# Optimization experiments

Hardware: AMD Instinct MI355X
Metric: run time of the kernel (lower is better)

Reference implementation:

```python
import jax, jax.numpy as jnp
import numpy as np

B, L, H, S2V = 32, 1024, 256, 256
STEP = 1          # HP_SLSTM_step window size
EPS = 1e-3        # LayerNorm eps (added to std, torch-style unbiased std)
NUM_LAYERS = 4
# LayerNorm param row indices in ln_a/ln_b:
# 0..5 -> word gates f1,f2,f3,f4,i,o ; 6 gd ; 7 go ; 8 gf ; 9 gi ; 10 gg


def _ln(x, a, b):
    # torch LayerNorm variant: unbiased std, eps added to std (not var)
    mean = x.mean(-1, keepdims=True)
    d = x - mean
    std = jnp.sqrt((d * d).sum(-1, keepdims=True) / (x.shape[-1] - 1))
    return a * d / (std + EPS) + b


def setup_inputs() -> dict:
    key = jax.random.key(0)
    ks = jax.random.split(key, 16)
    p = lambda k, shp: 0.1 * jax.random.normal(k, shp, dtype=jnp.float32)
    return {
        "word_inputs": jax.random.normal(ks[0], (B, L, H), dtype=jnp.float32),
        "sent_embeddings": jax.random.normal(ks[1], (B, S2V), dtype=jnp.float32),
        "mask": jnp.ones((B, L), dtype=jnp.float32),
        "h0": jax.random.uniform(ks[2], (B, L, H), minval=-0.05, maxval=0.05, dtype=jnp.float32),
        "c0": jax.random.uniform(ks[3], (B, L, H), minval=-0.05, maxval=0.05, dtype=jnp.float32),
        "Wx_g": p(ks[4], (6, H, H)),
        "Wh_g": p(ks[5], (6, 2 * H, H)),
        "Wi_g": p(ks[6], (6, H, H)),
        "Wd_g": p(ks[7], (6, H, H)),
        "b_g": p(ks[8], (6, H)),
        "gWx": p(ks[9], (4, H, H)),   # dummy gates d,i,o,f
        "gWh": p(ks[10], (4, H, H)),
        "gWg": p(ks[11], (4, S2V, H)),  # d,i,o,g
        "gb": p(ks[12], (4, H)),
        "ln_a": jnp.ones((11, H), dtype=jnp.float32),
        "ln_b": jnp.zeros((11, H), dtype=jnp.float32),
        "num_layers": NUM_LAYERS,
    }


def _win_sums(t):
    # sum of left-shifted (before) and right-shifted (after) neighbor states
    bef = jnp.zeros_like(t)
    aft = jnp.zeros_like(t)
    for s in range(1, STEP + 1):
        bef = bef + jnp.pad(t[:, :-s], ((0, 0), (s, 0), (0, 0)))
        aft = aft + jnp.pad(t[:, s:], ((0, 0), (0, s), (0, 0)))
    return bef.reshape(-1, t.shape[-1]), aft.reshape(-1, t.shape[-1])


def reference(word_inputs, sent_embeddings, mask, h0, c0, Wx_g, Wh_g, Wi_g,
              Wd_g, b_g, gWx, gWh, gWg, gb, ln_a, ln_b, num_layers):
    Bs, Ls, Hs = word_inputs.shape
    seq_mask = mask[..., None]                      # (B,L,1)
    msm = (mask * 1e25 - 1e25)[..., None]           # softmax mask (B,L,1)
    emb_h = (word_inputs * seq_mask).reshape(-1, Hs)  # fixed word embedding states
    emb_c = emb_h
    h = h0 * seq_mask
    c = c0 * seq_mask
    dh = h.mean(axis=1)                             # dummy (sentence) node (B,H)
    dc = c.mean(axis=1)

    for _ in range(num_layers):
        comb = h.mean(axis=1)                       # (B,H)
        rh = h.reshape(-1, Hs)                      # (B*L,H)
        tdh = (dh[:, None, :] * seq_mask).reshape(-1, Hs)
        tdc = (dc[:, None, :] * seq_mask).reshape(-1, Hs)

        # --- dummy (sentence-level) node gates ---
        gd = jax.nn.sigmoid(_ln(dh @ gWx[0] + sent_embeddings @ gWg[0] + comb @ gWh[0] + gb[0], ln_a[6], ln_b[6]))
        gi = jax.nn.sigmoid(_ln(dh @ gWx[1] + sent_embeddings @ gWg[1] + comb @ gWh[1], ln_a[9], ln_b[9]) + gb[1])  # bias outside LN, as in source
        gg = sent_embeddings @ gWg[3]
        go = jax.nn.sigmoid(_ln(dh @ gWx[2] + sent_embeddings @ gWg[2] + comb @ gWh[2] + gb[2], ln_a[7], ln_b[7]))
        gf = jax.nn.sigmoid(_ln(tdh @ gWx[3] + rh @ gWh[3] + gb[3], ln_a[8], ln_b[8]))
        gf = gf.reshape(Bs, Ls, Hs) + msm
        scores = jax.nn.softmax(jnp.concatenate([gf, gd[:, None, :], gi[:, None, :]], axis=1), axis=1)
        f_w = scores[:, :Ls]
        d_w = scores[:, Ls]
        i_w = scores[:, Ls + 1]
        dc_new = jnp.sum(f_w * c, axis=1) + d_w * dc + i_w * jnp.tanh(_ln(gg, ln_a[10], ln_b[10]))
        dh_new = go * jnp.tanh(dc_new)

        # --- word node gates (windowed message passing) ---
        hb, ha = _win_sums(h)
        cb, ca = _win_sums(c)
        cat_h = jnp.concatenate([hb, ha], axis=1)   # (B*L, 2H)
        pre = (jnp.einsum('nh,ghk->gnk', emb_h, Wx_g)
               + jnp.einsum('nc,gck->gnk', cat_h, Wh_g)
               + jnp.einsum('nh,ghk->gnk', rh, Wi_g)
               + jnp.einsum('nh,ghk->gnk', tdh, Wd_g)
               + b_g[:, None, :])                   # (6, B*L, H)
        gates = jax.nn.sigmoid(_ln(pre, ln_a[:6, None, :], ln_b[:6, None, :]))
        five = jax.nn.softmax(gates[:5], axis=0)    # normalize f1..f4,i
        f1, f2, f3, f4, i_t = five
        o_t = gates[5]
        c_new = cb * f1 + ca * f2 + emb_c * f3 + tdc * f4 + c.reshape(-1, Hs) * i_t
        h_new = o_t * jnp.tanh(c_new)
        h = h_new.reshape(Bs, Ls, Hs) * seq_mask
        c = c_new.reshape(Bs, Ls, Hs) * seq_mask
        dh, dc = dh_new, dc_new
    return h
```

## Files before the change

### kernel.cpp

```cpp
#include <hip/hip_runtime.h>
#include <cstddef>

#define Bz 32
#define Lz 1024
#define Hz 256
#define Nz (Bz*Lz)
#define NHz ((size_t)Nz*Hz)
#define BHz (Bz*Hz)
#define EPSz 1e-3f
#define NLAYERS 4
#define NCH 64
#define NTC 112
#define CHR 16384

typedef __bf16 bf8_t __attribute__((ext_vector_type(8)));
typedef __bf16 bf4_t __attribute__((ext_vector_type(4)));
typedef float  f4_t  __attribute__((ext_vector_type(4)));

__device__ inline float sigmoidf(float x){ return 1.f/(1.f+expf(-x)); }
__device__ inline float fsig(float x){ return __builtin_amdgcn_rcpf(1.f + __expf(-x)); }
__device__ inline float ftanh(float x){ return 1.f - 2.f*__builtin_amdgcn_rcpf(__expf(2.f*x)+1.f); }

template<int C>
__device__ inline float dppadd(float v){
  int t = __builtin_amdgcn_update_dpp(0, __builtin_bit_cast(int, v), C, 0xf, 0xf, true);
  return v + __builtin_bit_cast(float, t);
}
__device__ inline float dppsum16(float v){
  v = dppadd<0x111>(v);
  v = dppadd<0x112>(v);
  v = dppadd<0x114>(v);
  v = dppadd<0x118>(v);
  return v;
}

__device__ inline void gl_lds16(const void* g, void* l){
  __builtin_amdgcn_global_load_lds(
      (const __attribute__((address_space(1))) void*)g,
      (__attribute__((address_space(3))) void*)l, 16, 0, 0);
}

__device__ inline float2 block_sum2(float a, float b, float* red){
  #pragma unroll
  for (int off=32; off; off>>=1){ a += __shfl_down(a,off,64); b += __shfl_down(b,off,64); }
  int w = threadIdx.x>>6;
  __syncthreads();
  if ((threadIdx.x&63)==0){ red[w]=a; red[4+w]=b; }
  __syncthreads();
  return make_float2(red[0]+red[1]+red[2]+red[3], red[4]+red[5]+red[6]+red[7]);
}

__device__ inline float ln_block(float v, const float* la, const float* lb, int t, float* red){
  float2 ss = block_sum2(v, v*v, red);
  float mean = ss.x*(1.f/Hz);
  float var  = (ss.y - (float)Hz*mean*mean)*(1.f/(Hz-1));
  float isd  = 1.f/(sqrtf(fmaxf(var,0.f))+EPSz);
  return la[t]*(v-mean)*isd + lb[t];
}

__global__ void k_initb(const float* __restrict__ word, const float* __restrict__ h0,
                        const float* __restrict__ c0, const float* __restrict__ mask,
                        __bf16* __restrict__ xe, __bf16* __restrict__ h, __bf16* __restrict__ c){
  int tid = blockIdx.x*256 + threadIdx.x;
  int n = tid >> 5; int c8 = (tid & 31)*8;
  float m = mask[n];
  size_t off = (size_t)n*Hz + c8;
  const float4* wv = (const float4*)(word + off);
  float4 w0 = wv[0], w1 = wv[1];
  bf8_t o;
  o[0]=(__bf16)(w0.x*m); o[1]=(__bf16)(w0.y*m); o[2]=(__bf16)(w0.z*m); o[3]=(__bf16)(w0.w*m);
  o[4]=(__bf16)(w1.x*m); o[5]=(__bf16)(w1.y*m); o[6]=(__bf16)(w1.z*m); o[7]=(__bf16)(w1.w*m);
  *(bf8_t*)(xe + off) = o;
  const float4* hv = (const float4*)(h0 + off);
  float4 a0 = hv[0], a1 = hv[1];
  o[0]=(__bf16)(a0.x*m); o[1]=(__bf16)(a0.y*m); o[2]=(__bf16)(a0.z*m); o[3]=(__bf16)(a0.w*m);
  o[4]=(__bf16)(a1.x*m); o[5]=(__bf16)(a1.y*m); o[6]=(__bf16)(a1.z*m); o[7]=(__bf16)(a1.w*m);
  *(bf8_t*)(h + off) = o;
  const float4* cv = (const float4*)(c0 + off);
  float4 b0 = cv[0], b1 = cv[1];
  o[0]=(__bf16)(b0.x*m); o[1]=(__bf16)(b0.y*m); o[2]=(__bf16)(b0.z*m); o[3]=(__bf16)(b0.w*m);
  o[4]=(__bf16)(b1.x*m); o[5]=(__bf16)(b1.y*m); o[6]=(__bf16)(b1.z*m); o[7]=(__bf16)(b1.w*m);
  *(bf8_t*)(c + off) = o;
}

__global__ void k_packWt(const float* __restrict__ Wx, const float* __restrict__ Wh,
                         const float* __restrict__ Wi, const float* __restrict__ gWh3,
                         __bf16* __restrict__ Wt, __bf16* __restrict__ zbuf){
  int tid = blockIdx.x*256 + threadIdx.x;
  if (tid < 128) zbuf[tid] = (__bf16)0.f;
  int col = tid >> 7;
  int k0  = (tid & 127) << 3;
  if (col >= 1792) return;
  int g = col >> 8, cg = col & 255;
  int seg = k0 >> 8, kl0 = k0 & 255;
  bf8_t o;
  #pragma unroll
  for (int j=0;j<8;j++){
    int kl = kl0 + j;
    float v = 0.f;
    if (g < 6){
      if (seg==0)      v = Wx[((size_t)g*256 + kl)*256 + cg];
      else if (seg==1) v = Wh[((size_t)g*512 + kl)*256 + cg];
      else if (seg==2) v = Wh[((size_t)g*512 + 256 + kl)*256 + cg];
      else             v = Wi[((size_t)g*256 + kl)*256 + cg];
    } else {
      if (seg==3)      v = gWh3[(size_t)kl*256 + cg];
    }
    o[j] = (__bf16)v;
  }
  *(bf8_t*)(Wt + (size_t)col*1024 + k0) = o;
}

__global__ void k_meanpb(const __bf16* __restrict__ x, float* __restrict__ part){
  int b = blockIdx.x, ch = blockIdx.y, t = threadIdx.x;
  const __bf16* p = x + ((size_t)b*Lz + ch*128)*Hz + t;
  float s = 0.f;
  #pragma unroll 4
  for (int l=0;l<128;l++) s += (float)p[(size_t)l*Hz];
  part[(b*8+ch)*Hz + t] = s;
}
__global__ void k_comb8(const float* __restrict__ part, float* __restrict__ o){
  int b = blockIdx.x, t = threadIdx.x;
  float s = 0.f;
  #pragma unroll
  for (int ch=0;ch<8;ch++) s += part[(b*8+ch)*Hz + t];
  o[b*Hz+t] = s*(1.f/Lz);
}

__global__ __launch_bounds__(256) void k_small(
    const float* __restrict__ dh, const float* __restrict__ comb, const float* __restrict__ sent,
    const float* __restrict__ gWx, const float* __restrict__ gWh, const float* __restrict__ gWg,
    const float* __restrict__ gb, const float* __restrict__ Wd_g,
    const float* __restrict__ ln_a, const float* __restrict__ ln_b,
    float* __restrict__ gd, float* __restrict__ gi, float* __restrict__ go,
    float* __restrict__ tgg, float* __restrict__ dhWd7){
  int b = blockIdx.x, which = blockIdx.y, t = threadIdx.x;
  __shared__ float sdh[Hz], sse[Hz], sco[Hz];
  __shared__ float red[8];
  sdh[t]=dh[b*Hz+t]; sse[t]=sent[b*Hz+t]; sco[t]=comb[b*Hz+t];
  __syncthreads();
  float acc=0.f;
  if (which < 3){
    const float* W0 = gWx + which*Hz*Hz;
    const float* W1 = gWg + which*Hz*Hz;
    const float* W2 = gWh + which*Hz*Hz;
    for (int k=0;k<Hz;k++) acc += sdh[k]*W0[k*Hz+t] + sse[k]*W1[k*Hz+t] + sco[k]*W2[k*Hz+t];
    if (which==0){
      float r = ln_block(acc + gb[0*Hz+t], ln_a+6*Hz, ln_b+6*Hz, t, red);
      gd[b*Hz+t] = sigmoidf(r);
    } else if (which==1){
      float r = ln_block(acc, ln_a+9*Hz, ln_b+9*Hz, t, red);
      gi[b*Hz+t] = sigmoidf(r + gb[1*Hz+t]);
    } else {
      float r = ln_block(acc + gb[2*Hz+t], ln_a+7*Hz, ln_b+7*Hz, t, red);
      go[b*Hz+t] = sigmoidf(r);
    }
  } else if (which == 3){
    const float* W = gWg + 3*Hz*Hz;
    for (int k=0;k<Hz;k++) acc += sse[k]*W[k*Hz+t];
    float r = ln_block(acc, ln_a+10*Hz, ln_b+10*Hz, t, red);
    tgg[b*Hz+t] = tanhf(r);
  } else if (which == 4){
    const float* W = gWx + 3*Hz*Hz;
    for (int k=0;k<Hz;k++) acc += sdh[k]*W[k*Hz+t];
    dhWd7[(6*Bz + b)*Hz + t] = acc;
  } else {
    int g = which-5;
    const float* W = Wd_g + g*Hz*Hz;
    for (int k=0;k<Hz;k++) acc += sdh[k]*W[k*Hz+t];
    dhWd7[(g*Bz + b)*Hz + t] = acc;
  }
}

__global__ __launch_bounds__(256) void k_gemm(
    const __bf16* __restrict__ xe, const __bf16* __restrict__ h,
    const __bf16* __restrict__ Wt, const __bf16* __restrict__ zbuf,
    __bf16* __restrict__ pre, int n_base){
  __shared__ __align__(16) __bf16 sA[2][128*64];
  __shared__ __align__(16) __bf16 sB[2][128*64];
  int t = threadIdx.x;
  int w = t>>6, lane = t&63;
  int m16 = lane&15, p = lane>>4;
  int bx = blockIdx.x, by = blockIdx.y;
  int row0 = n_base + bx*128;
  int coltile = by*128;

  f4_t acc[4][4];
  #pragma unroll
  for (int i=0;i<4;i++)
    #pragma unroll
    for (int j=0;j<4;j++) acc[i][j] = (f4_t){0.f,0.f,0.f,0.f};

  int srr = t>>3;
  int sck = t&7;
  int arow = (w&1)*64 + m16;
  int brow = (w>>1)*64 + m16;
  int swz  = m16 & 7;

  auto STAGE = [&](int kk, int buf){
    int seg = kk>>2;
    int kloc = (kk&3)*64;
    #pragma unroll
    for (int it=0; it<4; ++it){
      int drow = it*32 + srr;
      int sc = (sck ^ (drow&7)) << 3;
      int r = row0 + drow;
      const __bf16* asrc;
      if (seg==0)      asrc = xe + (size_t)r*Hz + kloc + sc;
      else if (seg==3) asrc = h + (size_t)r*Hz + kloc + sc;
      else if (seg==1) asrc = ((r&1023)==0)    ? zbuf : h + ((size_t)(r-1)*Hz + kloc + sc);
      else             asrc = ((r&1023)==1023) ? zbuf : h + ((size_t)(r+1)*Hz + kloc + sc);
      gl_lds16(asrc, &sA[buf][drow*64 + sck*8]);
      const __bf16* bsrc = Wt + (size_t)(coltile + drow)*1024 + seg*256 + kloc + sc;
      gl_lds16(bsrc, &sB[buf][drow*64 + sck*8]);
    }
  };

  int kk_s = (by >= 12) ? 12 : 0;
  STAGE(kk_s, 0);
  __syncthreads();
  int cur = 0;
  #pragma unroll 1
  for (int kk=kk_s; kk<16; ++kk){
    if (kk < 15) STAGE(kk+1, cur^1);
    const char* Ab = (const char*)sA[cur];
    const char* Bb = (const char*)sB[cur];
    #pragma unroll
    for (int kb=0; kb<2; ++kb){
      bf8_t a[4], bb[4];
      int cofs = ((kb*4 + p) ^ swz) << 4;
      #pragma unroll
      for (int tr=0;tr<4;tr++)
        a[tr] = *(const bf8_t*)(Ab + (arow + tr*16)*128 + cofs);
      #pragma unroll
      for (int tc=0;tc<4;tc++)
        bb[tc] = *(const bf8_t*)(Bb + (brow + tc*16)*128 + cofs);
      #pragma unroll
      for (int tr=0;tr<4;tr++)
        #pragma unroll
        for (int tc=0;tc<4;tc++)
          acc[tr][tc] = __builtin_amdgcn_mfma_f32_16x16x32_bf16(a[tr], bb[tc], acc[tr][tc], 0, 0, 0);
    }
    __syncthreads();
    cur ^= 1;
  }

  int trg0 = (bx*128 + (w&1)*64) >> 4;
  int tcg0 = (coltile + (w>>1)*64) >> 4;
  #pragma unroll
  for (int tr=0;tr<4;tr++){
    #pragma unroll
    for (int tc=0;tc<4;tc++){
      size_t tile = (size_t)(trg0+tr)*NTC + (tcg0+tc);
      bf4_t o;
      o[0]=(__bf16)acc[tr][tc][0]; o[1]=(__bf16)acc[tr][tc][1];
      o[2]=(__bf16)acc[tr][tc][2]; o[3]=(__bf16)acc[tr][tc][3];
      *(bf4_t*)(pre + tile*256 + lane*4) = o;
    }
  }
}

__global__ __launch_bounds__(1024) void k_epi(
    const __bf16* __restrict__ pre, const __bf16* __restrict__ xe,
    const __bf16* __restrict__ cc, const float* __restrict__ mask,
    const float* __restrict__ dhWd7, const float* __restrict__ b_g,
    const float* __restrict__ gb3, const float* __restrict__ ln_a, const float* __restrict__ ln_b,
    const float* __restrict__ dc,
    float* __restrict__ outf, __bf16* __restrict__ hn, __bf16* __restrict__ cn,
    float* __restrict__ pm, float* __restrict__ ps, float* __restrict__ pn,
    int n_base, int last){
  __shared__ float sred_s[16][7][16];
  __shared__ float sred_q[16][7][16];
  __shared__ float smean[7][16];
  __shared__ float sisd[7][16];
  __shared__ float hsh[16*260];
  int t = threadIdx.x;
  int n0 = n_base + blockIdx.x*16;
  int b = n0 >> 10;
  int w16 = t>>6, lane = t&63, m16 = lane&15, p = lane>>4;
  int col = w16*16 + m16;
  size_t trk = blockIdx.x;

  bf4_t pv[7];
  float wd[7], bg[7], la[7], lb[7];
  #pragma unroll
  for (int g=0; g<7; ++g){
    size_t tile = trk*NTC + g*16 + w16;
    pv[g] = *(const bf4_t*)(pre + tile*256 + lane*4);
    wd[g] = dhWd7[(g*Bz + b)*Hz + col];
    bg[g] = (g<6) ? b_g[g*Hz + col] : gb3[col];
    int lnr = (g<6) ? g : 8;
    la[g] = ln_a[lnr*Hz+col]; lb[g] = ln_b[lnr*Hz+col];
  }
  float msk4[4], cvv[4], cb4[4], ca4[4], em4[4];
  #pragma unroll
  for (int reg=0; reg<4; ++reg){
    int n2 = n0 + p*4 + reg;
    int l2 = n2 & 1023;
    msk4[reg] = mask[n2];
    cvv[reg] = (float)cc[(size_t)n2*Hz + col];
    cb4[reg] = (l2==0)    ? 0.f : (float)cc[(size_t)(n2-1)*Hz + col];
    ca4[reg] = (l2==1023) ? 0.f : (float)cc[(size_t)(n2+1)*Hz + col];
    em4[reg] = (float)xe[(size_t)n2*Hz + col];
  }
  float tdc = dc[b*Hz + col];

  float acc[7][4];
  #pragma unroll
  for (int g=0; g<7; ++g){
    float s_r[4], q_r[4];
    #pragma unroll
    for (int reg=0; reg<4; ++reg){
      float x = (float)pv[g][reg] + msk4[reg]*wd[g] + bg[g];
      acc[g][reg] = x;
      s_r[reg] = dppsum16(x);
      q_r[reg] = dppsum16(x*x);
    }
    if (m16==15){
      #pragma unroll
      for (int reg=0; reg<4; ++reg){
        sred_s[w16][g][p*4+reg] = s_r[reg];
        sred_q[w16][g][p*4+reg] = q_r[reg];
      }
    }
  }
  __syncthreads();

  if (t < 112){
    int g = t>>4, row = t&15;
    float ss=0.f, qq=0.f;
    #pragma unroll
    for (int ww=0; ww<16; ++ww){
      ss += sred_s[ww][g][row];
      qq += sred_q[ww][g][row];
    }
    float mean = ss*(1.f/Hz);
    float var  = (qq - (float)Hz*mean*mean)*(1.f/(Hz-1));
    smean[g][row] = mean;
    sisd[g][row]  = __builtin_amdgcn_rcpf(sqrtf(fmaxf(var,0.f))+EPSz);
  }
  __syncthreads();

  #pragma unroll
  for (int g=0; g<7; ++g){
    #pragma unroll
    for (int reg=0; reg<4; ++reg){
      int row = p*4+reg;
      acc[g][reg] = fsig(la[g]*(acc[g][reg]-smean[g][row])*sisd[g][row] + lb[g]);
    }
  }

  {
    float mm = -1e30f, gfv[4];
    #pragma unroll
    for (int reg=0; reg<4; ++reg){
      float gv = acc[6][reg] + (msk4[reg]*1e25f - 1e25f);
      gfv[reg] = gv;
      mm = fmaxf(mm, gv);
    }
    float ss=0.f, nn=0.f;
    #pragma unroll
    for (int reg=0; reg<4; ++reg){
      float e = __expf(gfv[reg]-mm);
      ss += e; nn += e*cvv[reg];
    }
    #pragma unroll
    for (int off=16; off<64; off<<=1){
      float mo = __shfl_xor(mm, off, 64);
      float so = __shfl_xor(ss, off, 64);
      float no = __shfl_xor(nn, off, 64);
      float mN = fmaxf(mm, mo);
      float ea = __expf(mm-mN), eb = __expf(mo-mN);
      ss = ss*ea + so*eb; nn = nn*ea + no*eb; mm = mN;
    }
    if (p==0){
      int ch = (n0 >> 4) & (NCH-1);
      int idx = (b*NCH + ch)*Hz + col;
      pm[idx]=mm; ps[idx]=ss; pn[idx]=nn;
    }
  }

  float cnv[4];
  #pragma unroll
  for (int reg=0; reg<4; ++reg){
    float msk = msk4[reg];
    float g0=acc[0][reg], g1=acc[1][reg], g2=acc[2][reg], g3=acc[3][reg], g4=acc[4][reg];
    float m5 = fmaxf(fmaxf(fmaxf(g0,g1),fmaxf(g2,g3)),g4);
    float e0=__expf(g0-m5), e1=__expf(g1-m5), e2=__expf(g2-m5), e3=__expf(g3-m5), e4=__expf(g4-m5);
    float inv = __builtin_amdgcn_rcpf(e0+e1+e2+e3+e4);
    float cnew = (cb4[reg]*e0 + ca4[reg]*e1 + em4[reg]*e2 + (tdc*msk)*e3 + cvv[reg]*e4)*inv;
    float hv = acc[5][reg]*ftanh(cnew);
    hsh[(p*4+reg)*260 + col] = hv*msk;
    cnv[reg] = cnew*msk;
  }
  __syncthreads();
  {
    int row = t>>6, c4 = lane*4;
    int n = n0 + row;
    const float* src = hsh + row*260 + c4;
    float v0=src[0], v1=src[1], v2=src[2], v3=src[3];
    if (last){
      *(float4*)(outf + (size_t)n*Hz + c4) = make_float4(v0,v1,v2,v3);
    } else {
      bf4_t o; o[0]=(__bf16)v0; o[1]=(__bf16)v1; o[2]=(__bf16)v2; o[3]=(__bf16)v3;
      *(bf4_t*)(hn + (size_t)n*Hz + c4) = o;
    }
  }
  __syncthreads();
  #pragma unroll
  for (int reg=0; reg<4; ++reg) hsh[(p*4+reg)*260 + col] = cnv[reg];
  __syncthreads();
  {
    int row = t>>6, c4 = lane*4;
    const float* src = hsh + row*260 + c4;
    bf4_t o; o[0]=(__bf16)src[0]; o[1]=(__bf16)src[1]; o[2]=(__bf16)src[2]; o[3]=(__bf16)src[3];
    *(bf4_t*)(cn + (size_t)(n0+row)*Hz + c4) = o;
  }
}

__global__ void k_soft_comb(const float* __restrict__ pm, const float* __restrict__ ps,
    const float* __restrict__ pn,
    const float* __restrict__ gd, const float* __restrict__ gi, const float* __restrict__ go,
    const float* __restrict__ tgg, const float* __restrict__ dc,
    float* __restrict__ dc_new, float* __restrict__ dh_new){
  int b = blockIdx.x, t = threadIdx.x;
  float vgd = gd[b*Hz+t], vgi = gi[b*Hz+t];
  float m = fmaxf(vgd, vgi);
  for (int ch=0; ch<NCH; ch++) m = fmaxf(m, pm[(b*NCH+ch)*Hz + t]);
  float ed = expf(vgd - m), ei = expf(vgi - m);
  float s  = ed + ei;
  float num = ed*dc[b*Hz+t] + ei*tgg[b*Hz+t];
  for (int ch=0; ch<NCH; ch++){
    int idx = (b*NCH+ch)*Hz + t;
    float e = expf(pm[idx] - m);
    s   += ps[idx]*e;
    num += pn[idx]*e;
  }
  float dcn = num/s;
  dc_new[b*Hz+t] = dcn;
  dh_new[b*Hz+t] = go[b*Hz+t]*tanhf(dcn);
}

extern "C" void kernel_launch(void* const* d_in, const int* in_sizes, int n_in,
                              void* d_out, int out_size, void* d_ws, size_t ws_size,
                              hipStream_t stream) {
  const float* word  = (const float*)d_in[0];
  const float* sent  = (const float*)d_in[1];
  const float* mask  = (const float*)d_in[2];
  const float* h0    = (const float*)d_in[3];
  const float* c0    = (const float*)d_in[4];
  const float* Wx_g  = (const float*)d_in[5];
  const float* Wh_g  = (const float*)d_in[6];
  const float* Wi_g  = (const float*)d_in[7];
  const float* Wd_g  = (const float*)d_in[8];
  const float* b_g   = (const float*)d_in[9];
  const float* gWx   = (const float*)d_in[10];
  const float* gWh   = (const float*)d_in[11];
  const float* gWg   = (const float*)d_in[12];
  const float* gb    = (const float*)d_in[13];
  const float* ln_a  = (const float*)d_in[14];
  const float* ln_b  = (const float*)d_in[15];
  float* out = (float*)d_out;

  char* wc = (char*)d_ws;
  __bf16* xe  = (__bf16*)wc;  wc += NHz*2;
  __bf16* h_a = (__bf16*)wc;  wc += NHz*2;
  __bf16* h_b = (__bf16*)wc;  wc += NHz*2;
  __bf16* c_a = (__bf16*)wc;  wc += NHz*2;
  __bf16* c_b = (__bf16*)wc;  wc += NHz*2;
  __bf16* pre = (__bf16*)wc;  wc += (size_t)(CHR/16)*NTC*256*2;
  __bf16* Wt  = (__bf16*)wc;  wc += (size_t)1792*1024*2;
  __bf16* zbuf = (__bf16*)wc; wc += 256;
  float* dh_a = (float*)wc;   wc += BHz*4;
  float* dh_b = (float*)wc;   wc += BHz*4;
  float* dc_a = (float*)wc;   wc += BHz*4;
  float* dc_b = (float*)wc;   wc += BHz*4;
  float* comb = (float*)wc;   wc += BHz*4;
  float* gd   = (float*)wc;   wc += BHz*4;
  float* gi_  = (float*)wc;   wc += BHz*4;
  float* go_  = (float*)wc;   wc += BHz*4;
  float* tgg  = (float*)wc;   wc += BHz*4;
  float* dhWd7 = (float*)wc;  wc += 7*BHz*4;
  float* pmean = (float*)wc;  wc += 8*BHz*4;
  float* pm = (float*)wc;     wc += (size_t)Bz*NCH*Hz*4;
  float* ps = (float*)wc;     wc += (size_t)Bz*NCH*Hz*4;
  float* pn = (float*)wc;     wc += (size_t)Bz*NCH*Hz*4;

  k_packWt<<<896, 256, 0, stream>>>(Wx_g, Wh_g, Wi_g, gWh + 3*Hz*Hz, Wt, zbuf);
  k_initb<<<4096, 256, 0, stream>>>(word, h0, c0, mask, xe, h_a, c_a);
  k_meanpb<<<dim3(Bz,8), 256, 0, stream>>>(h_a, pmean);
  k_comb8<<<Bz, 256, 0, stream>>>(pmean, dh_a);
  k_meanpb<<<dim3(Bz,8), 256, 0, stream>>>(c_a, pmean);
  k_comb8<<<Bz, 256, 0, stream>>>(pmean, dc_a);

  __bf16* hc=h_a; __bf16* hn=h_b;
  __bf16* cc=c_a; __bf16* cn=c_b;
  float* dhc=dh_a; float* dcc=dc_a; float* dhn=dh_b; float* dcn=dc_b;

  for (int layer=0; layer<NLAYERS; ++layer){
    k_meanpb<<<dim3(Bz,8), 256, 0, stream>>>(hc, pmean);
    k_comb8<<<Bz, 256, 0, stream>>>(pmean, comb);
    k_small<<<dim3(Bz,11), 256, 0, stream>>>(dhc, comb, sent, gWx, gWh, gWg, gb, Wd_g,
                                             ln_a, ln_b, gd, gi_, go_, tgg, dhWd7);
    int last = (layer == NLAYERS-1) ? 1 : 0;
    for (int chunk=0; chunk<Nz/CHR; ++chunk){
      int n_base = chunk*CHR;
      k_gemm<<<dim3(CHR/128, 14), 256, 0, stream>>>(xe, hc, Wt, zbuf, pre, n_base);
      k_epi<<<CHR/16, 1024, 0, stream>>>(pre, xe, cc, mask, dhWd7, b_g, gb + 3*Hz,
                                         ln_a, ln_b, dcc, out, hn, cn, pm, ps, pn,
                                         n_base, last);
    }
    k_soft_comb<<<Bz, 256, 0, stream>>>(pm, ps, pn, gd, gi_, go_, tgg, dcc, dcn, dhn);
    __bf16* tb;
    tb=hc; hc=hn; hn=tb;
    tb=cc; cc=cn; cn=tb;
    float* tmp;
    tmp=dhc; dhc=dhn; dhn=tmp;
    tmp=dcc; dcc=dcn; dcn=tmp;
  }
  (void)in_sizes; (void)n_in; (void)out_size; (void)ws_size;
}
```

Measured before the change: 1.383 ms.

## Enlarge GEMM block tile to 256x256 with 512 threads and MFMA priority

The gate GEMM moves from 128x128 tiles with 256 threads to 256x256 tiles with 512 threads. Each wave now computes a 128x64 sub-tile, and the B fragments are loaded once per k-step and reused across four A row pairs. The column-tile special case that skips the first k-tiles is remapped to the new tiling. s_setprio is raised around the MFMA bursts. The goal is higher arithmetic intensity and less global and LDS traffic per FLOP. The cost is 128KB of LDS, a larger register footprint and far fewer blocks per launch (448 instead of 1792), which may hurt occupancy and load balance.

```diff
diff --git a/kernel.cpp b/kernel.cpp
--- a/kernel.cpp
+++ b/kernel.cpp
@@ -172,37 +172,37 @@
   }
 }
 
-__global__ __launch_bounds__(256) void k_gemm(
+__global__ __launch_bounds__(512) void k_gemm(
     const __bf16* __restrict__ xe, const __bf16* __restrict__ h,
     const __bf16* __restrict__ Wt, const __bf16* __restrict__ zbuf,
     __bf16* __restrict__ pre, int n_base){
-  __shared__ __align__(16) __bf16 sA[2][128*64];
-  __shared__ __align__(16) __bf16 sB[2][128*64];
+  __shared__ __align__(16) __bf16 sA[2][256*64];
+  __shared__ __align__(16) __bf16 sB[2][256*64];
   int t = threadIdx.x;
   int w = t>>6, lane = t&63;
   int m16 = lane&15, p = lane>>4;
   int bx = blockIdx.x, by = blockIdx.y;
-  int row0 = n_base + bx*128;
-  int coltile = by*128;
-
-  f4_t acc[4][4];
-  #pragma unroll
-  for (int i=0;i<4;i++)
+  int row0 = n_base + bx*256;
+  int coltile = by*256;
+
+  f4_t acc[8][4];
+  #pragma unroll
+  for (int i=0;i<8;i++)
     #pragma unroll
     for (int j=0;j<4;j++) acc[i][j] = (f4_t){0.f,0.f,0.f,0.f};
 
   int srr = t>>3;
   int sck = t&7;
-  int arow = (w&1)*64 + m16;
-  int brow = (w>>1)*64 + m16;
+  int arow = (w>>2)*128 + m16;
+  int brow = (w&3)*64 + m16;
   int swz  = m16 & 7;
 
-  auto STAGE = [&](int kk, int buf){
-    int seg = kk>>2;
-    int kloc = (kk&3)*64;
+  auto STAGE = [&](int kt, int buf){
+    int seg = kt>>2;
+    int kloc = (kt&3)*64;
     #pragma unroll
     for (int it=0; it<4; ++it){
-      int drow = it*32 + srr;
+      int drow = it*64 + srr;
       int sc = (sck ^ (drow&7)) << 3;
       int r = row0 + drow;
       const __bf16* asrc;
@@ -216,39 +216,51 @@
     }
   };
 
-  int kk_s = (by >= 12) ? 12 : 0;
-  STAGE(kk_s, 0);
+  int kt_s = (by==6) ? 12 : 0;
+  STAGE(kt_s, 0);
   __syncthreads();
   int cur = 0;
   #pragma unroll 1
-  for (int kk=kk_s; kk<16; ++kk){
-    if (kk < 15) STAGE(kk+1, cur^1);
+  for (int kt=kt_s; kt<16; ++kt){
+    if (kt < 15) STAGE(kt+1, cur^1);
     const char* Ab = (const char*)sA[cur];
     const char* Bb = (const char*)sB[cur];
-    #pragma unroll
-    for (int kb=0; kb<2; ++kb){
-      bf8_t a[4], bb[4];
-      int cofs = ((kb*4 + p) ^ swz) << 4;
+    bf8_t bb[4][2];
+    #pragma unroll
+    for (int tc=0;tc<4;tc++)
       #pragma unroll
-      for (int tr=0;tr<4;tr++)
-        a[tr] = *(const bf8_t*)(Ab + (arow + tr*16)*128 + cofs);
+      for (int kb=0;kb<2;kb++){
+        int cofs = ((kb*4 + p) ^ swz) << 4;
+        bb[tc][kb] = *(const bf8_t*)(Bb + (brow + tc*16)*128 + cofs);
+      }
+    #pragma unroll
+    for (int q=0; q<4; ++q){
+      bf8_t a[2][2];
       #pragma unroll
-      for (int tc=0;tc<4;tc++)
-        bb[tc] = *(const bf8_t*)(Bb + (brow + tc*16)*128 + cofs);
+      for (int i=0;i<2;i++)
+        #pragma unroll
+        for (int kb=0;kb<2;kb++){
+          int cofs = ((kb*4 + p) ^ swz) << 4;
+          a[i][kb] = *(const bf8_t*)(Ab + (arow + (q*2+i)*16)*128 + cofs);
+        }
+      __builtin_amdgcn_s_setprio(1);
       #pragma unroll
-      for (int tr=0;tr<4;tr++)
+      for (int i=0;i<2;i++)
         #pragma unroll
         for (int tc=0;tc<4;tc++)
-          acc[tr][tc] = __builtin_amdgcn_mfma_f32_16x16x32_bf16(a[tr], bb[tc], acc[tr][tc], 0, 0, 0);
+          #pragma unroll
+          for (int kb=0;kb<2;kb++)
+            acc[q*2+i][tc] = __builtin_amdgcn_mfma_f32_16x16x32_bf16(a[i][kb], bb[tc][kb], acc[q*2+i][tc], 0, 0, 0);
+      __builtin_amdgcn_s_setprio(0);
     }
     __syncthreads();
     cur ^= 1;
   }
 
-  int trg0 = (bx*128 + (w&1)*64) >> 4;
-  int tcg0 = (coltile + (w>>1)*64) >> 4;
-  #pragma unroll
-  for (int tr=0;tr<4;tr++){
+  int trg0 = (bx*256 + (w>>2)*128) >> 4;
+  int tcg0 = (coltile + (w&3)*64) >> 4;
+  #pragma unroll
+  for (int tr=0;tr<8;tr++){
     #pragma unroll
     for (int tc=0;tc<4;tc++){
       size_t tile = (size_t)(trg0+tr)*NTC + (tcg0+tc);
@@ -505,7 +517,7 @@
     int last = (layer == NLAYERS-1) ? 1 : 0;
     for (int chunk=0; chunk<Nz/CHR; ++chunk){
       int n_base = chunk*CHR;
-      k_gemm<<<dim3(CHR/128, 14), 256, 0, stream>>>(xe, hc, Wt, zbuf, pre, n_base);
+      k_gemm<<<dim3(CHR/256, 7), 512, 0, stream>>>(xe, hc, Wt, zbuf, pre, n_base);
       k_epi<<<CHR/16, 1024, 0, stream>>>(pre, xe, cc, mask, dhWd7, b_g, gb + 3*Hz,
                                          ln_a, ln_b, dcc, out, hn, cn, pm, ps, pn,
                                          n_base, last);
```

Measured after the change: 1.409 ms. No clear change (+1.9%).
